# Kernel optimization log

Measured on AMD Instinct MI355X. Metric: run time of the kernel, lower is better.

## Reference

```python
import jax, jax.numpy as jnp
import numpy as np

B, N, F, A = 8, 2048, 512, 512  # batch, n_dim (tokens), feature_dim, attention_dim
BN_EPS = 1e-5


def setup_inputs() -> dict:
    key = jax.random.key(0)
    ks = jax.random.split(key, 9)
    s_f = 1.0 / np.sqrt(F)
    s_a = 1.0 / np.sqrt(A)
    return {
        "x": jax.random.normal(ks[0], (B, N, F), dtype=jnp.float32),
        "Wq": jax.random.uniform(ks[1], (A, F), jnp.float32, -s_f, s_f),
        "bq": jax.random.uniform(ks[2], (A,), jnp.float32, -s_f, s_f),
        "Wk": jax.random.uniform(ks[3], (A, F), jnp.float32, -s_f, s_f),
        "bk": jax.random.uniform(ks[4], (A,), jnp.float32, -s_f, s_f),
        "Wv": jax.random.uniform(ks[5], (A, F), jnp.float32, -s_f, s_f),
        "bv": jax.random.uniform(ks[6], (A,), jnp.float32, -s_f, s_f),
        "Wo": jax.random.uniform(ks[7], (F, A), jnp.float32, -s_a, s_a),
        "bo": jax.random.uniform(ks[8], (F,), jnp.float32, -s_a, s_a),
        "gamma": jnp.ones((N,), dtype=jnp.float32),
        "beta": jnp.zeros((N,), dtype=jnp.float32),
    }


def reference(x, Wq, bq, Wk, bk, Wv, bv, Wo, bo, gamma, beta):
    # QKV projections: [B,N,F] -> [B,N,A]
    q = jnp.einsum("bnf,af->bna", x, Wq) + bq
    k = jnp.einsum("bnf,af->bna", x, Wk) + bk
    v = jnp.einsum("bnf,af->bna", x, Wv) + bv
    # unscaled single-head attention (no 1/sqrt(d) factor, matches source)
    scores = jnp.einsum("bna,bma->bnm", q, k)          # [B,N,N]
    weights = jax.nn.softmax(scores, axis=-1)
    feature = jnp.einsum("bnm,bma->bna", weights, v)    # [B,N,A]
    # LBR: Linear -> BatchNorm1d(n_dim) over channel dim N -> ReLU
    lin = jnp.einsum("bna,fa->bnf", feature, Wo) + bo   # [B,N,F]
    mean = jnp.mean(lin, axis=(0, 2), keepdims=True)    # stats over batch+last dim
    var = jnp.mean(jnp.square(lin - mean), axis=(0, 2), keepdims=True)  # biased var
    bn = gamma[None, :, None] * (lin - mean) * jax.lax.rsqrt(var + BN_EPS) + beta[None, :, None]
    return jax.nn.relu(bn) + x
```

## Files before the change

kernel.cpp:

```cpp
#include <hip/hip_runtime.h>
#include <hip/hip_fp16.h>
#include <stdint.h>

#define B_   8
#define N_   2048
#define F_   512
#define A_   512
#define MTOT (B_ * N_)

typedef unsigned short u16;
typedef unsigned int   u32;
typedef __attribute__((ext_vector_type(8))) __bf16    bf16x8;
typedef __attribute__((ext_vector_type(8))) _Float16  f16x8;
typedef __attribute__((ext_vector_type(4))) float     f32x4;

__device__ __forceinline__ u16 f2bf(float f) {
    u32 u = __builtin_bit_cast(u32, f);
    u32 r = u + 0x7fffu + ((u >> 16) & 1u);
    return (u16)(r >> 16);
}
__device__ __forceinline__ u16 f2h(float f) {
    _Float16 h = (_Float16)f;
    return __builtin_bit_cast(u16, h);
}

__device__ __forceinline__ void gload_lds16(const u16* g, u16* l) {
    __builtin_amdgcn_global_load_lds(
        (const __attribute__((address_space(1))) u32*)(const u32*)g,
        (__attribute__((address_space(3))) u32*)(u32*)l,
        16, 0, 0);
}

template <int FMT>
__global__ __launch_bounds__(256) void cvt16(const float* __restrict__ in,
                                             u16* __restrict__ out, int n4) {
    int i = blockIdx.x * 256 + threadIdx.x;
    if (i >= n4) return;
    float4 v = ((const float4*)in)[i];
    u32 a, b;
    if constexpr (FMT == 0) {
        a = (u32)f2bf(v.x) | ((u32)f2bf(v.y) << 16);
        b = (u32)f2bf(v.z) | ((u32)f2bf(v.w) << 16);
    } else {
        a = (u32)f2h(v.x) | ((u32)f2h(v.y) << 16);
        b = (u32)f2h(v.z) | ((u32)f2h(v.w) << 16);
    }
    ((uint2*)out)[i] = make_uint2(a, b);
}

template <int BIAS_MODE, int OUT_FMT, int IN_FMT>
__global__ __launch_bounds__(256)
void gemm_nt(const u16* __restrict__ A, int lda, long sA,
             const u16* __restrict__ Bm, int ldb, long sB,
             const float* __restrict__ bias,
             void* __restrict__ Cv, int ldc, long sC, int K)
{
    __shared__ alignas(16) u16 lA[128 * 64];
    __shared__ alignas(16) u16 lB[128 * 64];

    const int z = blockIdx.z;
    A  += (long)z * sA;
    Bm += (long)z * sB;

    const int m0 = blockIdx.x * 128;
    const int n0 = blockIdx.y * 128;
    const int t = threadIdx.x;
    const int lane = t & 63, wave = t >> 6;
    const int wr = (wave >> 1) * 64;
    const int wc = (wave & 1) * 64;
    const int frow = lane & 15;
    const int fk   = (lane >> 4) * 8;

    f32x4 acc[4][4];
#pragma unroll
    for (int i = 0; i < 4; i++)
#pragma unroll
        for (int j = 0; j < 4; j++)
#pragma unroll
            for (int r = 0; r < 4; r++) acc[i][j][r] = 0.f;

    const int srow = t >> 3;
    const int scol = (t & 7) * 8;

    for (int kt = 0; kt < K; kt += 64) {
        __syncthreads();
#pragma unroll
        for (int s = 0; s < 4; ++s) {
            int row = s * 32 + srow;
            const u16* ga = A  + (long)(m0 + row) * lda + (kt + scol);
            const u16* gb = Bm + (long)(n0 + row) * ldb + (kt + scol);
            gload_lds16(ga, &lA[s * 2048 + t * 8]);
            gload_lds16(gb, &lB[s * 2048 + t * 8]);
        }
        __syncthreads();
#pragma unroll
        for (int kk = 0; kk < 64; kk += 32) {
            uint4 ar[4], br[4];
#pragma unroll
            for (int i = 0; i < 4; i++)
                ar[i] = *(const uint4*)&lA[(wr + i * 16 + frow) * 64 + kk + fk];
#pragma unroll
            for (int j = 0; j < 4; j++)
                br[j] = *(const uint4*)&lB[(wc + j * 16 + frow) * 64 + kk + fk];
#pragma unroll
            for (int i = 0; i < 4; i++)
#pragma unroll
                for (int j = 0; j < 4; j++) {
                    if constexpr (IN_FMT == 0)
                        acc[i][j] = __builtin_amdgcn_mfma_f32_16x16x32_bf16(
                            __builtin_bit_cast(bf16x8, ar[i]),
                            __builtin_bit_cast(bf16x8, br[j]),
                            acc[i][j], 0, 0, 0);
                    else
                        acc[i][j] = __builtin_amdgcn_mfma_f32_16x16x32_f16(
                            __builtin_bit_cast(f16x8, ar[i]),
                            __builtin_bit_cast(f16x8, br[j]),
                            acc[i][j], 0, 0, 0);
                }
        }
    }

    const int rbase = (lane >> 4) * 4;
#pragma unroll
    for (int i = 0; i < 4; i++) {
        int m = m0 + wr + i * 16 + rbase;
#pragma unroll
        for (int j = 0; j < 4; j++) {
            int n = n0 + wc + j * 16 + frow;
            float badd = 0.f;
            if (BIAS_MODE == 1) badd = bias[n];
#pragma unroll
            for (int r = 0; r < 4; r++) {
                float v = acc[i][j][r];
                if (BIAS_MODE == 1) v += badd;
                if (BIAS_MODE == 2) v += bias[m + r];
                long idx = (long)(m + r) * ldc + n + (long)z * sC;
                if constexpr (OUT_FMT == 0) {
                    ((u16*)Cv)[idx] = f2bf(v);
                } else if constexpr (OUT_FMT == 1) {
                    ((float*)Cv)[idx] = v;
                } else {
                    ((u16*)Cv)[idx] = f2h(v);
                }
            }
        }
    }
}

__global__ __launch_bounds__(256) void softmax_rows(u16* __restrict__ S) {
    __shared__ float red[16];
    const long row = blockIdx.x;
    u16* p = S + row * (long)N_;
    const int t = threadIdx.x;
    const int lane = t & 63, wave = t >> 6;

    uint4 raw = ((const uint4*)p)[t];
    const __half2* hp = (const __half2*)&raw;
    float v[8];
#pragma unroll
    for (int j = 0; j < 4; j++) {
        float2 f = __half22float2(hp[j]);
        v[2 * j]     = f.x;
        v[2 * j + 1] = f.y;
    }
    float mx = v[0];
#pragma unroll
    for (int j = 1; j < 8; j++) mx = fmaxf(mx, v[j]);
#pragma unroll
    for (int o = 32; o; o >>= 1) mx = fmaxf(mx, __shfl_xor(mx, o));
    if (lane == 0) red[wave] = mx;
    __syncthreads();
    mx = fmaxf(fmaxf(red[0], red[1]), fmaxf(red[2], red[3]));

    float s = 0.f;
#pragma unroll
    for (int j = 0; j < 8; j++) { v[j] = __expf(v[j] - mx); s += v[j]; }
#pragma unroll
    for (int o = 32; o; o >>= 1) s += __shfl_xor(s, o);
    if (lane == 0) red[8 + wave] = s;
    __syncthreads();
    s = red[8] + red[9] + red[10] + red[11];
    float inv = 1.f / s;
    u32 w[4];
#pragma unroll
    for (int j = 0; j < 4; j++) {
        u32 lo = f2bf(v[2 * j] * inv);
        u32 hi = f2bf(v[2 * j + 1] * inv);
        w[j] = lo | (hi << 16);
    }
    ((uint4*)p)[t] = make_uint4(w[0], w[1], w[2], w[3]);
}

__global__ __launch_bounds__(256) void bn_stats(const float* __restrict__ lin,
                                                float* __restrict__ stats) {
    __shared__ float red[16];
    const int n = blockIdx.x;
    const int t = threadIdx.x;
    const int lane = t & 63, wave = t >> 6;
    float s = 0.f, s2 = 0.f;
    for (int idx = t; idx < 1024; idx += 256) {
        int b = idx >> 7, f4 = idx & 127;
        float4 x = ((const float4*)(lin + ((long)b * N_ + n) * F_))[f4];
        s  += x.x + x.y + x.z + x.w;
        s2 += x.x * x.x + x.y * x.y + x.z * x.z + x.w * x.w;
    }
#pragma unroll
    for (int o = 32; o; o >>= 1) { s += __shfl_xor(s, o); s2 += __shfl_xor(s2, o); }
    if (lane == 0) { red[wave] = s; red[8 + wave] = s2; }
    __syncthreads();
    if (t == 0) {
        float S1 = red[0] + red[1] + red[2] + red[3];
        float S2 = red[8] + red[9] + red[10] + red[11];
        float mean = S1 / 4096.f;
        float var  = S2 / 4096.f - mean * mean;
        stats[n]      = mean;
        stats[N_ + n] = rsqrtf(var + 1e-5f);
    }
}

__global__ __launch_bounds__(256)
void bn_relu_add(const float* __restrict__ lin, const float* __restrict__ x,
                 const float* __restrict__ gamma, const float* __restrict__ beta,
                 const float* __restrict__ stats, float* __restrict__ out) {
    long i4 = (long)blockIdx.x * 256 + threadIdx.x;
    int n = (int)((i4 >> 7) & (N_ - 1));
    float mean = stats[n], rstd = stats[N_ + n];
    float scale = gamma[n] * rstd;
    float shift = beta[n] - mean * scale;
    float4 l  = ((const float4*)lin)[i4];
    float4 xx = ((const float4*)x)[i4];
    float4 o;
    o.x = fmaxf(l.x * scale + shift, 0.f) + xx.x;
    o.y = fmaxf(l.y * scale + shift, 0.f) + xx.y;
    o.z = fmaxf(l.z * scale + shift, 0.f) + xx.z;
    o.w = fmaxf(l.w * scale + shift, 0.f) + xx.w;
    ((float4*)out)[i4] = o;
}

extern "C" void kernel_launch(void* const* d_in, const int* in_sizes, int n_in,
                              void* d_out, int out_size, void* d_ws, size_t ws_size,
                              hipStream_t stream)
{
    (void)in_sizes; (void)n_in; (void)out_size; (void)ws_size;
    const float* x     = (const float*)d_in[0];
    const float* Wq    = (const float*)d_in[1];
    const float* bq    = (const float*)d_in[2];
    const float* Wk    = (const float*)d_in[3];
    const float* bk    = (const float*)d_in[4];
    const float* Wv    = (const float*)d_in[5];
    const float* bv    = (const float*)d_in[6];
    const float* Wo    = (const float*)d_in[7];
    const float* bo    = (const float*)d_in[8];
    const float* gamma = (const float*)d_in[9];
    const float* beta  = (const float*)d_in[10];
    float* out = (float*)d_out;
    char*  ws  = (char*)d_ws;

    const size_t MB = 1024 * 1024;
    u16*   wqkh  = (u16*)(ws + 0);
    u16*   wvh   = (u16*)(ws + 1 * MB);
    u16*   wob   = (u16*)(ws + 1 * MB + 512 * 1024);
    float* stats = (float*)(ws + 2 * MB);
    float* bqk   = (float*)(ws + 2 * MB + 64 * 1024);
    u16*   xh    = (u16*)(ws + 4 * MB);
    u16*   qkh   = (u16*)(ws + 20 * MB);
    u16*   vt    = (u16*)(ws + 52 * MB);
    u16*   S     = (u16*)(ws + 68 * MB);
    u16*   feat  = (u16*)(ws + 132 * MB);
    float* lin   = (float*)(ws + 148 * MB);

    hipMemcpyAsync(bqk,       bq, 512 * sizeof(float), hipMemcpyDeviceToDevice, stream);
    hipMemcpyAsync(bqk + 512, bk, 512 * sizeof(float), hipMemcpyDeviceToDevice, stream);

    cvt16<1><<<8192, 256, 0, stream>>>(x,  xh,  2097152);
    cvt16<1><<<256,  256, 0, stream>>>(Wq, wqkh,          65536);
    cvt16<1><<<256,  256, 0, stream>>>(Wk, wqkh + 262144, 65536);
    cvt16<1><<<256,  256, 0, stream>>>(Wv, wvh, 65536);
    cvt16<0><<<256,  256, 0, stream>>>(Wo, wob, 65536);

    gemm_nt<1, 2, 1><<<dim3(128, 8, 1), 256, 0, stream>>>(
        xh, 512, 0, wqkh, 512, 0, bqk, qkh, 1024, 0, 512);
    gemm_nt<2, 0, 1><<<dim3(4, 128, 1), 256, 0, stream>>>(
        wvh, 512, 0, xh, 512, 0, bv, vt, MTOT, 0, 512);

    gemm_nt<0, 2, 1><<<dim3(16, 16, 8), 256, 0, stream>>>(
        qkh, 1024, (long)N_ * 1024,
        qkh + 512, 1024, (long)N_ * 1024,
        nullptr, S, N_, (long)N_ * N_, 512);
    softmax_rows<<<MTOT, 256, 0, stream>>>(S);
    gemm_nt<0, 0, 0><<<dim3(16, 4, 8), 256, 0, stream>>>(
        S, N_, (long)N_ * N_,
        vt, MTOT, (long)N_,
        nullptr, feat, A_, (long)N_ * A_, 2048);

    gemm_nt<1, 1, 0><<<dim3(128, 4, 1), 256, 0, stream>>>(
        feat, 512, 0, wob, 512, 0, bo, lin, 512, 0, 512);
    bn_stats<<<2048, 256, 0, stream>>>(lin, stats);
    bn_relu_add<<<8192, 256, 0, stream>>>(lin, x, gamma, beta, stats, out);
}
```

Baseline: 245.6 us.

## Add 8-wave 256x256 pipelined fp16 GEMM for QK projection and scores

Introduces a new 512-thread GEMM kernel with 256x256 output tiles, a 4-stage LDS ring buffer fed by direct global-to-LDS loads, explicit vmcnt waits, and interleaved MFMA halves with priority bumps. It replaces the generic 128x128 GEMM for the fused Q/K projection and the batched QK^T score computation. The aim is more data reuse per tile and better overlap of memory loads with MFMA work. In exchange it uses 128KB of LDS and many accumulator registers, which limits occupancy to one block per CU and gives a coarser grid.

```diff
diff --git a/kernel.cpp b/kernel.cpp
--- a/kernel.cpp
+++ b/kernel.cpp
@@ -46,6 +46,119 @@
         b = (u32)f2h(v.z) | ((u32)f2h(v.w) << 16);
     }
     ((uint2*)out)[i] = make_uint2(a, b);
+}
+
+template <int BIAS_MODE>
+__global__ __launch_bounds__(512)
+void gemm8p(const u16* __restrict__ A, int lda, long sA,
+            const u16* __restrict__ Bm, int ldb, long sB,
+            const float* __restrict__ bias,
+            u16* __restrict__ C, int ldc, long sC, int K)
+{
+    __shared__ alignas(16) u16 lds8[65536];
+
+    const int z = blockIdx.z;
+    const int m0 = blockIdx.x * 256;
+    const int n0 = blockIdx.y * 256;
+    const u16* Ag = A  + (long)z * sA + (long)m0 * lda;
+    const u16* Bg = Bm + (long)z * sB + (long)n0 * ldb;
+
+    const int t = threadIdx.x;
+    const int lane = t & 63, wave = t >> 6;
+    const int wm = wave >> 2;
+    const int wn = wave & 3;
+    const int frow = lane & 15;
+    const int fkel = (lane >> 4) * 8;
+
+    const int NT = K >> 5;
+
+    auto stage2 = [&](const u16* g, int ld, int kel, u16* lbase) {
+#pragma unroll
+        for (int r = 0; r < 2; ++r) {
+            int row = r * 128 + (t >> 2);
+            int cel = ((t & 3) * 8) ^ ((row & 3) << 3);
+            gload_lds16(g + (long)row * ld + kel + cel, lbase + r * 4096 + t * 8);
+        }
+    };
+    auto rd = [&](int base, int row) -> uint4 {
+        return *(const uint4*)&lds8[base + row * 32 + (fkel ^ ((row & 3) << 3))];
+    };
+
+    f32x4 acc[8][4];
+#pragma unroll
+    for (int i = 0; i < 8; i++)
+#pragma unroll
+        for (int j = 0; j < 4; j++)
+#pragma unroll
+            for (int r = 0; r < 4; r++) acc[i][j][r] = 0.f;
+
+#pragma unroll
+    for (int T = 0; T < 3; ++T) {
+        stage2(Ag, lda, T * 32, &lds8[T * 16384]);
+        stage2(Bg, ldb, T * 32, &lds8[T * 16384 + 8192]);
+    }
+
+    for (int T = 0; T < NT; ++T) {
+        const int s  = (T & 3) * 16384;
+        const int sn = ((T + 3) & 3) * 16384;
+        const bool st = (T + 3 < NT);
+        const int kel = (T + 3) * 32;
+
+        if (T < NT - 2)      asm volatile("s_waitcnt vmcnt(8)" ::: "memory");
+        else if (T == NT - 2) asm volatile("s_waitcnt vmcnt(4)" ::: "memory");
+        else                 asm volatile("s_waitcnt vmcnt(0)" ::: "memory");
+        __builtin_amdgcn_sched_barrier(0);
+        __builtin_amdgcn_s_barrier();
+        __builtin_amdgcn_sched_barrier(0);
+
+        uint4 ar[4], br[4];
+#pragma unroll
+        for (int i = 0; i < 4; i++) ar[i] = rd(s, wm * 128 + i * 16 + frow);
+#pragma unroll
+        for (int j = 0; j < 4; j++) br[j] = rd(s + 8192, wn * 64 + j * 16 + frow);
+        if (st) stage2(Ag, lda, kel, &lds8[sn]);
+        __builtin_amdgcn_s_setprio(1);
+#pragma unroll
+        for (int i = 0; i < 4; i++)
+#pragma unroll
+            for (int j = 0; j < 4; j++)
+                acc[i][j] = __builtin_amdgcn_mfma_f32_16x16x32_f16(
+                    __builtin_bit_cast(f16x8, ar[i]),
+                    __builtin_bit_cast(f16x8, br[j]), acc[i][j], 0, 0, 0);
+        __builtin_amdgcn_s_setprio(0);
+        __builtin_amdgcn_sched_barrier(0);
+        __builtin_amdgcn_s_barrier();
+        __builtin_amdgcn_sched_barrier(0);
+
+        uint4 ar2[4];
+#pragma unroll
+        for (int i = 0; i < 4; i++) ar2[i] = rd(s, wm * 128 + 64 + i * 16 + frow);
+        if (st) stage2(Bg, ldb, kel, &lds8[sn + 8192]);
+        __builtin_amdgcn_s_setprio(1);
+#pragma unroll
+        for (int i = 0; i < 4; i++)
+#pragma unroll
+            for (int j = 0; j < 4; j++)
+                acc[4 + i][j] = __builtin_amdgcn_mfma_f32_16x16x32_f16(
+                    __builtin_bit_cast(f16x8, ar2[i]),
+                    __builtin_bit_cast(f16x8, br[j]), acc[4 + i][j], 0, 0, 0);
+        __builtin_amdgcn_s_setprio(0);
+    }
+
+    const int q4 = (lane >> 4) * 4;
+#pragma unroll
+    for (int ii = 0; ii < 8; ii++) {
+        int m = m0 + wm * 128 + (ii >> 2) * 64 + (ii & 3) * 16 + q4;
+#pragma unroll
+        for (int j = 0; j < 4; j++) {
+            int n = n0 + wn * 64 + j * 16 + frow;
+            float badd = 0.f;
+            if (BIAS_MODE == 1) badd = bias[n];
+#pragma unroll
+            for (int r = 0; r < 4; r++)
+                C[(long)(m + r) * ldc + n + (long)z * sC] = f2h(acc[ii][j][r] + badd);
+        }
+    }
 }
 
 template <int BIAS_MODE, int OUT_FMT, int IN_FMT>
@@ -278,12 +391,12 @@
     cvt16<1><<<256,  256, 0, stream>>>(Wv, wvh, 65536);
     cvt16<0><<<256,  256, 0, stream>>>(Wo, wob, 65536);
 
-    gemm_nt<1, 2, 1><<<dim3(128, 8, 1), 256, 0, stream>>>(
+    gemm8p<1><<<dim3(64, 4, 1), 512, 0, stream>>>(
         xh, 512, 0, wqkh, 512, 0, bqk, qkh, 1024, 0, 512);
     gemm_nt<2, 0, 1><<<dim3(4, 128, 1), 256, 0, stream>>>(
         wvh, 512, 0, xh, 512, 0, bv, vt, MTOT, 0, 512);
 
-    gemm_nt<0, 2, 1><<<dim3(16, 16, 8), 256, 0, stream>>>(
+    gemm8p<0><<<dim3(8, 8, 8), 512, 0, stream>>>(
         qkh, 1024, (long)N_ * 1024,
         qkh + 512, 1024, (long)N_ * 1024,
         nullptr, S, N_, (long)N_ * N_, 512);
```

Result: faster. 238.7 us (-2.8%).

## Replace GEMM with 256-row, 8-wave, double-buffered, swizzled LDS pipelined kernel

Applied to the files above, without the earlier changes.

Replaces the 128x128 single-buffered GEMM with a 512-thread kernel using 256xBN tiles, double-buffered LDS with an XOR swizzle, and staged global-to-LDS loads interleaved with MFMA phases under explicit vmcnt waits, barriers and setprio. The aim is to hide global-load latency, cut LDS bank conflicts and raise the compute-to-load ratio. The PV GEMM now folds the batch into M through a diagonal B offset instead of grid z. The risks are higher register and LDS pressure and fragile hand-tuned wait counts.

```diff
diff --git a/kernel.cpp b/kernel.cpp
--- a/kernel.cpp
+++ b/kernel.cpp
@@ -29,6 +29,19 @@
         (const __attribute__((address_space(1))) u32*)(const u32*)g,
         (__attribute__((address_space(3))) u32*)(u32*)l,
         16, 0, 0);
+}
+
+#define VMCNT(n) asm volatile("s_waitcnt vmcnt(" #n ")" ::: "memory")
+
+__device__ __forceinline__ void sync_pre() {
+    __builtin_amdgcn_sched_barrier(0);
+    __builtin_amdgcn_s_barrier();
+    asm volatile("s_waitcnt lgkmcnt(0)" ::: "memory");
+    __builtin_amdgcn_sched_barrier(0);
+}
+__device__ __forceinline__ void sync_post() {
+    __builtin_amdgcn_sched_barrier(0);
+    __builtin_amdgcn_s_barrier();
 }
 
 template <int FMT>
@@ -48,100 +61,202 @@
     ((uint2*)out)[i] = make_uint2(a, b);
 }
 
-template <int BIAS_MODE, int OUT_FMT, int IN_FMT>
-__global__ __launch_bounds__(256)
-void gemm_nt(const u16* __restrict__ A, int lda, long sA,
-             const u16* __restrict__ Bm, int ldb, long sB,
-             const float* __restrict__ bias,
-             void* __restrict__ Cv, int ldc, long sC, int K)
+template <int BN, int BIAS_MODE, int OUT_FMT, int IN_FMT>
+__global__ __launch_bounds__(512, 2)
+void gemm8(const u16* __restrict__ A, int lda, long sA,
+           const u16* __restrict__ Bm, int ldb, long sB,
+           const float* __restrict__ bias,
+           void* __restrict__ Cv, int ldc, long sC, int K, int bdiag)
 {
-    __shared__ alignas(16) u16 lA[128 * 64];
-    __shared__ alignas(16) u16 lB[128 * 64];
-
-    const int z = blockIdx.z;
-    A  += (long)z * sA;
-    Bm += (long)z * sB;
-
-    const int m0 = blockIdx.x * 128;
-    const int n0 = blockIdx.y * 128;
+    constexpr int UNITS = (BN == 256) ? 4 : 3;
+    constexpr int NF = BN / 64;
+    __shared__ alignas(16) u16 lds[2 * UNITS * 8192];
+
+    const int z  = blockIdx.z;
+    const int m0 = blockIdx.x * 256;
+    const int n0 = blockIdx.y * BN;
+    const u16* Ag = A  + (long)z * sA + (long)m0 * lda;
+    const u16* Bg = Bm + (long)z * sB + (long)n0 * ldb + (long)(m0 >> 11) * bdiag;
+
     const int t = threadIdx.x;
-    const int lane = t & 63, wave = t >> 6;
-    const int wr = (wave >> 1) * 64;
-    const int wc = (wave & 1) * 64;
+    const int lane = t & 63;
+    const int wave = t >> 6;
+    const int wm = wave >> 2, wn = wave & 3;
     const int frow = lane & 15;
-    const int fk   = (lane >> 4) * 8;
-
-    f32x4 acc[4][4];
-#pragma unroll
-    for (int i = 0; i < 4; i++)
-#pragma unroll
-        for (int j = 0; j < 4; j++)
+    const int fk8 = (lane >> 4) * 8;
+
+    const int srr = t >> 3;
+    const int ses = ((t & 7) * 8) ^ ((srr & 7) << 3);
+
+    auto stageA = [&](int buf, int h, int kt) {
+        u16* dst = &lds[(buf * UNITS + h) * 8192 + t * 8];
+        const u16* g = Ag + kt * 64 + ses;
+        gload_lds16(g + (long)(srr + h * 64) * lda,        dst);
+        gload_lds16(g + (long)(srr + 128 + h * 64) * lda,  dst + 4096);
+    };
+    auto stageB = [&](int buf, int h, int kt) {
+        u16* dst = &lds[(buf * UNITS + 2 + h) * 8192 + t * 8];
+        const u16* g = Bg + kt * 64 + ses;
+        int R0;
+        if constexpr (BN == 256) R0 = (srr & 31) + ((srr >> 5) << 6) + h * 32;
+        else                     R0 = srr;
+        int R1 = R0 + ((BN == 256) ? 128 : 64);
+        gload_lds16(g + (long)R0 * ldb, dst);
+        gload_lds16(g + (long)R1 * ldb, dst + 4096);
+    };
+    auto rdA = [&](int buf, int q, int i, int ks) -> uint4 {
+        int rr = wm * 64 + i * 16 + frow;
+        int e  = (ks * 32 + fk8) ^ ((rr & 7) << 3);
+        return *(const uint4*)&lds[(buf * UNITS + q) * 8192 + rr * 64 + e];
+    };
+    auto rdB = [&](int buf, int p, int j, int ks) -> uint4 {
+        int rr = wn * 32 + j * 16 + frow;
+        int e  = (ks * 32 + fk8) ^ ((rr & 7) << 3);
+        return *(const uint4*)&lds[(buf * UNITS + 2 + p) * 8192 + rr * 64 + e];
+    };
+    auto MF = [&](uint4 a, uint4 b, f32x4 c) -> f32x4 {
+        if constexpr (IN_FMT == 0)
+            return __builtin_amdgcn_mfma_f32_16x16x32_bf16(
+                __builtin_bit_cast(bf16x8, a), __builtin_bit_cast(bf16x8, b), c, 0, 0, 0);
+        else
+            return __builtin_amdgcn_mfma_f32_16x16x32_f16(
+                __builtin_bit_cast(f16x8, a), __builtin_bit_cast(f16x8, b), c, 0, 0, 0);
+    };
+
+    f32x4 acc[8][NF];
+#pragma unroll
+    for (int i = 0; i < 8; i++)
+#pragma unroll
+        for (int j = 0; j < NF; j++)
 #pragma unroll
             for (int r = 0; r < 4; r++) acc[i][j][r] = 0.f;
 
-    const int srow = t >> 3;
-    const int scol = (t & 7) * 8;
-
-    for (int kt = 0; kt < K; kt += 64) {
-        __syncthreads();
-#pragma unroll
-        for (int s = 0; s < 4; ++s) {
-            int row = s * 32 + srow;
-            const u16* ga = A  + (long)(m0 + row) * lda + (kt + scol);
-            const u16* gb = Bm + (long)(n0 + row) * ldb + (kt + scol);
-            gload_lds16(ga, &lA[s * 2048 + t * 8]);
-            gload_lds16(gb, &lB[s * 2048 + t * 8]);
+    uint4 fa[4][2], fb0[2][2], fb1[2][2];
+    const int NT = K >> 6;
+
+    if constexpr (BN == 256) {
+        stageA(0, 0, 0); stageB(0, 0, 0); stageB(0, 1, 0); stageA(0, 1, 0);
+        VMCNT(4);
+    } else {
+        stageA(0, 0, 0); stageB(0, 0, 0); stageA(0, 1, 0);
+        VMCNT(2);
+    }
+    __builtin_amdgcn_sched_barrier(0);
+    __builtin_amdgcn_s_barrier();
+
+    for (int kt = 0; kt < NT; ++kt) {
+        const int buf = kt & 1, nb = buf ^ 1;
+        const bool st = (kt + 1 < NT);
+
+        if constexpr (BN == 256) {
+#pragma unroll
+            for (int i = 0; i < 4; i++) { fa[i][0] = rdA(buf, 0, i, 0); fa[i][1] = rdA(buf, 0, i, 1); }
+#pragma unroll
+            for (int j = 0; j < 2; j++) { fb0[j][0] = rdB(buf, 0, j, 0); fb0[j][1] = rdB(buf, 0, j, 1); }
+            if (st) { stageA(nb, 0, kt + 1); VMCNT(4); } else VMCNT(2);
+            sync_pre();
+            __builtin_amdgcn_s_setprio(1);
+#pragma unroll
+            for (int ks = 0; ks < 2; ks++)
+#pragma unroll
+                for (int i = 0; i < 4; i++)
+#pragma unroll
+                    for (int j = 0; j < 2; j++)
+                        acc[i][j] = MF(fa[i][ks], fb0[j][ks], acc[i][j]);
+            __builtin_amdgcn_s_setprio(0);
+            sync_post();
+#pragma unroll
+            for (int j = 0; j < 2; j++) { fb1[j][0] = rdB(buf, 1, j, 0); fb1[j][1] = rdB(buf, 1, j, 1); }
+            if (st) { stageB(nb, 0, kt + 1); VMCNT(4); } else VMCNT(0);
+            sync_pre();
+            __builtin_amdgcn_s_setprio(1);
+#pragma unroll
+            for (int ks = 0; ks < 2; ks++)
+#pragma unroll
+                for (int i = 0; i < 4; i++)
+#pragma unroll
+                    for (int j = 0; j < 2; j++)
+                        acc[i][2 + j] = MF(fa[i][ks], fb1[j][ks], acc[i][2 + j]);
+            __builtin_amdgcn_s_setprio(0);
+            sync_post();
+#pragma unroll
+            for (int i = 0; i < 4; i++) { fa[i][0] = rdA(buf, 1, i, 0); fa[i][1] = rdA(buf, 1, i, 1); }
+            if (st) stageB(nb, 1, kt + 1);
+            sync_pre();
+            __builtin_amdgcn_s_setprio(1);
+#pragma unroll
+            for (int ks = 0; ks < 2; ks++)
+#pragma unroll
+                for (int i = 0; i < 4; i++)
+#pragma unroll
+                    for (int j = 0; j < 2; j++)
+                        acc[4 + i][j] = MF(fa[i][ks], fb0[j][ks], acc[4 + i][j]);
+            __builtin_amdgcn_s_setprio(0);
+            sync_post();
+            if (st) { stageA(nb, 1, kt + 1); VMCNT(4); }
+            sync_pre();
+            __builtin_amdgcn_s_setprio(1);
+#pragma unroll
+            for (int ks = 0; ks < 2; ks++)
+#pragma unroll
+                for (int i = 0; i < 4; i++)
+#pragma unroll
+                    for (int j = 0; j < 2; j++)
+                        acc[4 + i][2 + j] = MF(fa[i][ks], fb1[j][ks], acc[4 + i][2 + j]);
+            __builtin_amdgcn_s_setprio(0);
+            sync_post();
+        } else {
+#pragma unroll
+            for (int i = 0; i < 4; i++) { fa[i][0] = rdA(buf, 0, i, 0); fa[i][1] = rdA(buf, 0, i, 1); }
+#pragma unroll
+            for (int j = 0; j < 2; j++) { fb0[j][0] = rdB(buf, 0, j, 0); fb0[j][1] = rdB(buf, 0, j, 1); }
+            if (st) { stageA(nb, 0, kt + 1); stageB(nb, 0, kt + 1); VMCNT(4); } else VMCNT(0);
+            sync_pre();
+            __builtin_amdgcn_s_setprio(1);
+#pragma unroll
+            for (int ks = 0; ks < 2; ks++)
+#pragma unroll
+                for (int i = 0; i < 4; i++)
+#pragma unroll
+                    for (int j = 0; j < 2; j++)
+                        acc[i][j] = MF(fa[i][ks], fb0[j][ks], acc[i][j]);
+            __builtin_amdgcn_s_setprio(0);
+            sync_post();
+#pragma unroll
+            for (int i = 0; i < 4; i++) { fa[i][0] = rdA(buf, 1, i, 0); fa[i][1] = rdA(buf, 1, i, 1); }
+            if (st) { stageA(nb, 1, kt + 1); VMCNT(2); }
+            sync_pre();
+            __builtin_amdgcn_s_setprio(1);
+#pragma unroll
+            for (int ks = 0; ks < 2; ks++)
+#pragma unroll
+                for (int i = 0; i < 4; i++)
+#pragma unroll
+                    for (int j = 0; j < 2; j++)
+                        acc[4 + i][j] = MF(fa[i][ks], fb0[j][ks], acc[4 + i][j]);
+            __builtin_amdgcn_s_setprio(0);
+            sync_post();
         }
-        __syncthreads();
-#pragma unroll
-        for (int kk = 0; kk < 64; kk += 32) {
-            uint4 ar[4], br[4];
-#pragma unroll
-            for (int i = 0; i < 4; i++)
-                ar[i] = *(const uint4*)&lA[(wr + i * 16 + frow) * 64 + kk + fk];
-#pragma unroll
-            for (int j = 0; j < 4; j++)
-                br[j] = *(const uint4*)&lB[(wc + j * 16 + frow) * 64 + kk + fk];
-#pragma unroll
-            for (int i = 0; i < 4; i++)
-#pragma unroll
-                for (int j = 0; j < 4; j++) {
-                    if constexpr (IN_FMT == 0)
-                        acc[i][j] = __builtin_amdgcn_mfma_f32_16x16x32_bf16(
-                            __builtin_bit_cast(bf16x8, ar[i]),
-                            __builtin_bit_cast(bf16x8, br[j]),
-                            acc[i][j], 0, 0, 0);
-                    else
-                        acc[i][j] = __builtin_amdgcn_mfma_f32_16x16x32_f16(
-                            __builtin_bit_cast(f16x8, ar[i]),
-                            __builtin_bit_cast(f16x8, br[j]),
-                            acc[i][j], 0, 0, 0);
-                }
-        }
-    }
-
-    const int rbase = (lane >> 4) * 4;
-#pragma unroll
-    for (int i = 0; i < 4; i++) {
-        int m = m0 + wr + i * 16 + rbase;
-#pragma unroll
-        for (int j = 0; j < 4; j++) {
-            int n = n0 + wc + j * 16 + frow;
+    }
+
+    const int rq = (lane >> 4) * 4;
+#pragma unroll
+    for (int am = 0; am < 8; am++) {
+        const int m = m0 + wm * 128 + (am >> 2) * 64 + (am & 3) * 16 + rq;
+#pragma unroll
+        for (int an = 0; an < NF; an++) {
+            const int n = n0 + wn * (BN / 4) + an * 16 + frow;
             float badd = 0.f;
             if (BIAS_MODE == 1) badd = bias[n];
 #pragma unroll
             for (int r = 0; r < 4; r++) {
-                float v = acc[i][j][r];
+                float v = acc[am][an][r];
                 if (BIAS_MODE == 1) v += badd;
                 if (BIAS_MODE == 2) v += bias[m + r];
                 long idx = (long)(m + r) * ldc + n + (long)z * sC;
-                if constexpr (OUT_FMT == 0) {
-                    ((u16*)Cv)[idx] = f2bf(v);
-                } else if constexpr (OUT_FMT == 1) {
-                    ((float*)Cv)[idx] = v;
-                } else {
-                    ((u16*)Cv)[idx] = f2h(v);
-                }
+                if constexpr (OUT_FMT == 0)      ((u16*)Cv)[idx] = f2bf(v);
+                else if constexpr (OUT_FMT == 1) ((float*)Cv)[idx] = v;
+                else                             ((u16*)Cv)[idx] = f2h(v);
             }
         }
     }
@@ -278,23 +393,19 @@
     cvt16<1><<<256,  256, 0, stream>>>(Wv, wvh, 65536);
     cvt16<0><<<256,  256, 0, stream>>>(Wo, wob, 65536);
 
-    gemm_nt<1, 2, 1><<<dim3(128, 8, 1), 256, 0, stream>>>(
-        xh, 512, 0, wqkh, 512, 0, bqk, qkh, 1024, 0, 512);
-    gemm_nt<2, 0, 1><<<dim3(4, 128, 1), 256, 0, stream>>>(
-        wvh, 512, 0, xh, 512, 0, bv, vt, MTOT, 0, 512);
-
-    gemm_nt<0, 2, 1><<<dim3(16, 16, 8), 256, 0, stream>>>(
-        qkh, 1024, (long)N_ * 1024,
-        qkh + 512, 1024, (long)N_ * 1024,
-        nullptr, S, N_, (long)N_ * N_, 512);
+    gemm8<256, 1, 2, 1><<<dim3(64, 4, 1), 512, 0, stream>>>(
+        xh, 512, 0, wqkh, 512, 0, bqk, qkh, 1024, 0, 512, 0);
+    gemm8<128, 2, 0, 1><<<dim3(2, 128, 1), 512, 0, stream>>>(
+        wvh, 512, 0, xh, 512, 0, bv, vt, MTOT, 0, 512, 0);
+    gemm8<256, 0, 2, 1><<<dim3(8, 8, 8), 512, 0, stream>>>(
+        qkh, 1024, (long)N_ * 1024, qkh + 512, 1024, (long)N_ * 1024,
+        nullptr, S, N_, (long)N_ * N_, 512, 0);
     softmax_rows<<<MTOT, 256, 0, stream>>>(S);
-    gemm_nt<0, 0, 0><<<dim3(16, 4, 8), 256, 0, stream>>>(
-        S, N_, (long)N_ * N_,
-        vt, MTOT, (long)N_,
-        nullptr, feat, A_, (long)N_ * A_, 2048);
-
-    gemm_nt<1, 1, 0><<<dim3(128, 4, 1), 256, 0, stream>>>(
-        feat, 512, 0, wob, 512, 0, bo, lin, 512, 0, 512);
+    gemm8<128, 0, 0, 0><<<dim3(64, 4, 1), 512, 0, stream>>>(
+        S, N_, 0, vt, MTOT, 0, nullptr, feat, A_, 0, 2048, 2048);
+    gemm8<128, 1, 1, 0><<<dim3(64, 4, 1), 512, 0, stream>>>(
+        feat, 512, 0, wob, 512, 0, bo, lin, 512, 0, 512, 0);
+
     bn_stats<<<2048, 256, 0, stream>>>(lin, stats);
     bn_relu_add<<<8192, 256, 0, stream>>>(lin, x, gamma, beta, stats, out);
 }
```

Result: faster. 214.2 us (-12.8%).

## Pipeline GEMM with triple-buffered LDS, swizzled layout, and fused BN stats

Applied to the files above, without the earlier changes.

Replaces the GEMM kernel with a triple-buffered, K-step-32 pipeline that keeps prefetching global-to-LDS loads in flight under explicit vmcnt waits. It also XOR-swizzles the LDS layout to reduce bank conflicts and changes the wave tiling so each wave owns 128x32. BatchNorm statistics are now accumulated in the output-projection GEMM epilogue with atomics, removing the separate bn_stats pass over lin. The attention-value GEMM batch index is folded into the grid via a diagonal offset. The trade-offs are more hand-tuned scheduling and atomic contention on the stats buffer.

```diff
diff --git a/kernel.cpp b/kernel.cpp
--- a/kernel.cpp
+++ b/kernel.cpp
@@ -30,6 +30,10 @@
         (__attribute__((address_space(3))) u32*)(u32*)l,
         16, 0, 0);
 }
+
+#define VMCNT(n) asm volatile("s_waitcnt vmcnt(" #n ")" ::: "memory")
+#define LGKM0()  asm volatile("s_waitcnt lgkmcnt(0)" ::: "memory")
+#define SCHEDB() __builtin_amdgcn_sched_barrier(0)
 
 template <int FMT>
 __global__ __launch_bounds__(256) void cvt16(const float* __restrict__ in,
@@ -48,99 +52,140 @@
     ((uint2*)out)[i] = make_uint2(a, b);
 }
 
-template <int BIAS_MODE, int OUT_FMT, int IN_FMT>
-__global__ __launch_bounds__(256)
-void gemm_nt(const u16* __restrict__ A, int lda, long sA,
-             const u16* __restrict__ Bm, int ldb, long sB,
-             const float* __restrict__ bias,
-             void* __restrict__ Cv, int ldc, long sC, int K)
+template <int BIAS_MODE, int OUT_FMT, int IN_FMT, int STATS>
+__global__ __launch_bounds__(256, 3)
+void gemmp(const u16* __restrict__ A, int lda, long sA,
+           const u16* __restrict__ Bm, int ldb, long sB,
+           const float* __restrict__ bias,
+           void* __restrict__ Cv, int ldc, long sC, int K, int bdiag,
+           float* __restrict__ stats)
 {
-    __shared__ alignas(16) u16 lA[128 * 64];
-    __shared__ alignas(16) u16 lB[128 * 64];
-
-    const int z = blockIdx.z;
-    A  += (long)z * sA;
-    Bm += (long)z * sB;
-
+    __shared__ alignas(16) u16 lds[3][2][4096];
+
+    const int z  = blockIdx.z;
     const int m0 = blockIdx.x * 128;
     const int n0 = blockIdx.y * 128;
+    const u16* Ag = A  + (long)z * sA + (long)m0 * lda;
+    const u16* Bg = Bm + (long)z * sB + (long)n0 * ldb + (long)(m0 >> 11) * bdiag;
+
     const int t = threadIdx.x;
-    const int lane = t & 63, wave = t >> 6;
-    const int wr = (wave >> 1) * 64;
-    const int wc = (wave & 1) * 64;
+    const int lane = t & 63;
+    const int wn   = t >> 6;
     const int frow = lane & 15;
-    const int fk   = (lane >> 4) * 8;
-
-    f32x4 acc[4][4];
-#pragma unroll
-    for (int i = 0; i < 4; i++)
-#pragma unroll
-        for (int j = 0; j < 4; j++)
+    const int fk8  = (lane >> 4) * 8;
+
+    const int sr = t >> 2;
+    const int se = ((t & 3) * 8) ^ ((sr & 3) << 3);
+
+    auto stage = [&](int slot, int unit, const u16* g, int ld, int kel) {
+        u16* dst = &lds[slot][unit][t * 8];
+        const u16* gp = g + kel + se;
+        gload_lds16(gp + (long)sr * ld,        dst);
+        gload_lds16(gp + (long)(sr + 64) * ld, dst + 2048);
+    };
+    auto rd = [&](int slot, int unit, int row) -> uint4 {
+        return *(const uint4*)&lds[slot][unit][row * 32 + (fk8 ^ ((row & 3) << 3))];
+    };
+    auto MF = [&](uint4 a, uint4 b, f32x4 c) -> f32x4 {
+        if constexpr (IN_FMT == 0)
+            return __builtin_amdgcn_mfma_f32_16x16x32_bf16(
+                __builtin_bit_cast(bf16x8, a), __builtin_bit_cast(bf16x8, b), c, 0, 0, 0);
+        else
+            return __builtin_amdgcn_mfma_f32_16x16x32_f16(
+                __builtin_bit_cast(f16x8, a), __builtin_bit_cast(f16x8, b), c, 0, 0, 0);
+    };
+
+    f32x4 acc[8][2];
+#pragma unroll
+    for (int i = 0; i < 8; i++)
+#pragma unroll
+        for (int j = 0; j < 2; j++)
 #pragma unroll
             for (int r = 0; r < 4; r++) acc[i][j][r] = 0.f;
 
-    const int srow = t >> 3;
-    const int scol = (t & 7) * 8;
-
-    for (int kt = 0; kt < K; kt += 64) {
-        __syncthreads();
-#pragma unroll
-        for (int s = 0; s < 4; ++s) {
-            int row = s * 32 + srow;
-            const u16* ga = A  + (long)(m0 + row) * lda + (kt + scol);
-            const u16* gb = Bm + (long)(n0 + row) * ldb + (kt + scol);
-            gload_lds16(ga, &lA[s * 2048 + t * 8]);
-            gload_lds16(gb, &lB[s * 2048 + t * 8]);
+    const int NT = K >> 5;
+
+    stage(0, 0, Ag, lda, 0);  stage(0, 1, Bg, ldb, 0);
+    stage(1, 0, Ag, lda, 32); stage(1, 1, Bg, ldb, 32);
+
+    int bc = 0, b1 = 1, b2 = 2;
+    uint4 fa[4], fb[2];
+
+    for (int kt = 0; kt < NT; ++kt) {
+        const bool st2 = (kt + 2 < NT);
+        const int kel2 = (kt + 2) << 5;
+
+        if (st2) {
+            stage(b2, 0, Ag, lda, kel2);
+            VMCNT(6);
+        } else if (kt + 2 == NT) {
+            VMCNT(4);
+        } else {
+            VMCNT(0);
         }
-        __syncthreads();
-#pragma unroll
-        for (int kk = 0; kk < 64; kk += 32) {
-            uint4 ar[4], br[4];
-#pragma unroll
-            for (int i = 0; i < 4; i++)
-                ar[i] = *(const uint4*)&lA[(wr + i * 16 + frow) * 64 + kk + fk];
-#pragma unroll
-            for (int j = 0; j < 4; j++)
-                br[j] = *(const uint4*)&lB[(wc + j * 16 + frow) * 64 + kk + fk];
-#pragma unroll
-            for (int i = 0; i < 4; i++)
-#pragma unroll
-                for (int j = 0; j < 4; j++) {
-                    if constexpr (IN_FMT == 0)
-                        acc[i][j] = __builtin_amdgcn_mfma_f32_16x16x32_bf16(
-                            __builtin_bit_cast(bf16x8, ar[i]),
-                            __builtin_bit_cast(bf16x8, br[j]),
-                            acc[i][j], 0, 0, 0);
-                    else
-                        acc[i][j] = __builtin_amdgcn_mfma_f32_16x16x32_f16(
-                            __builtin_bit_cast(f16x8, ar[i]),
-                            __builtin_bit_cast(f16x8, br[j]),
-                            acc[i][j], 0, 0, 0);
+        SCHEDB();
+        __builtin_amdgcn_s_barrier();
+        SCHEDB();
+#pragma unroll
+        for (int i = 0; i < 4; i++) fa[i] = rd(bc, 0, i * 16 + frow);
+        fb[0] = rd(bc, 1, wn * 32 + frow);
+        fb[1] = rd(bc, 1, wn * 32 + 16 + frow);
+        LGKM0(); SCHEDB();
+        __builtin_amdgcn_s_setprio(1);
+#pragma unroll
+        for (int i = 0; i < 4; i++)
+#pragma unroll
+            for (int j = 0; j < 2; j++)
+                acc[i][j] = MF(fa[i], fb[j], acc[i][j]);
+        __builtin_amdgcn_s_setprio(0);
+
+        if (st2) stage(b2, 1, Bg, ldb, kel2);
+#pragma unroll
+        for (int i = 0; i < 4; i++) fa[i] = rd(bc, 0, 64 + i * 16 + frow);
+        LGKM0(); SCHEDB();
+        __builtin_amdgcn_s_setprio(1);
+#pragma unroll
+        for (int i = 0; i < 4; i++)
+#pragma unroll
+            for (int j = 0; j < 2; j++)
+                acc[4 + i][j] = MF(fa[i], fb[j], acc[4 + i][j]);
+        __builtin_amdgcn_s_setprio(0);
+        SCHEDB();
+        __builtin_amdgcn_s_barrier();
+        int tmp = bc; bc = b1; b1 = b2; b2 = tmp;
+    }
+
+    const int rq = (lane >> 4) * 4;
+#pragma unroll
+    for (int am = 0; am < 8; am++) {
+        const int m = m0 + am * 16 + rq;
+#pragma unroll
+        for (int r = 0; r < 4; r++) {
+            float vv[2];
+#pragma unroll
+            for (int an = 0; an < 2; an++) {
+                const int n = n0 + wn * 32 + an * 16 + frow;
+                float v = acc[am][an][r];
+                if (BIAS_MODE == 1) v += bias[n];
+                if (BIAS_MODE == 2) v += bias[m + r];
+                vv[an] = v;
+                long idx = (long)(m + r) * ldc + n + (long)z * sC;
+                if constexpr (OUT_FMT == 0)      ((u16*)Cv)[idx] = f2bf(v);
+                else if constexpr (OUT_FMT == 1) ((float*)Cv)[idx] = v;
+                else                             ((u16*)Cv)[idx] = f2h(v);
+            }
+            if constexpr (STATS) {
+                float s1 = vv[0] + vv[1];
+                float s2 = vv[0] * vv[0] + vv[1] * vv[1];
+#pragma unroll
+                for (int o = 1; o < 16; o <<= 1) {
+                    s1 += __shfl_xor(s1, o);
+                    s2 += __shfl_xor(s2, o);
                 }
-        }
-    }
-
-    const int rbase = (lane >> 4) * 4;
-#pragma unroll
-    for (int i = 0; i < 4; i++) {
-        int m = m0 + wr + i * 16 + rbase;
-#pragma unroll
-        for (int j = 0; j < 4; j++) {
-            int n = n0 + wc + j * 16 + frow;
-            float badd = 0.f;
-            if (BIAS_MODE == 1) badd = bias[n];
-#pragma unroll
-            for (int r = 0; r < 4; r++) {
-                float v = acc[i][j][r];
-                if (BIAS_MODE == 1) v += badd;
-                if (BIAS_MODE == 2) v += bias[m + r];
-                long idx = (long)(m + r) * ldc + n + (long)z * sC;
-                if constexpr (OUT_FMT == 0) {
-                    ((u16*)Cv)[idx] = f2bf(v);
-                } else if constexpr (OUT_FMT == 1) {
-                    ((float*)Cv)[idx] = v;
-                } else {
-                    ((u16*)Cv)[idx] = f2h(v);
+                if (frow == 0) {
+                    int tok = (m + r) & (N_ - 1);
+                    atomicAdd(&stats[tok], s1);
+                    atomicAdd(&stats[N_ + tok], s2);
                 }
             }
         }
@@ -191,40 +236,15 @@
     ((uint4*)p)[t] = make_uint4(w[0], w[1], w[2], w[3]);
 }
 
-__global__ __launch_bounds__(256) void bn_stats(const float* __restrict__ lin,
-                                                float* __restrict__ stats) {
-    __shared__ float red[16];
-    const int n = blockIdx.x;
-    const int t = threadIdx.x;
-    const int lane = t & 63, wave = t >> 6;
-    float s = 0.f, s2 = 0.f;
-    for (int idx = t; idx < 1024; idx += 256) {
-        int b = idx >> 7, f4 = idx & 127;
-        float4 x = ((const float4*)(lin + ((long)b * N_ + n) * F_))[f4];
-        s  += x.x + x.y + x.z + x.w;
-        s2 += x.x * x.x + x.y * x.y + x.z * x.z + x.w * x.w;
-    }
-#pragma unroll
-    for (int o = 32; o; o >>= 1) { s += __shfl_xor(s, o); s2 += __shfl_xor(s2, o); }
-    if (lane == 0) { red[wave] = s; red[8 + wave] = s2; }
-    __syncthreads();
-    if (t == 0) {
-        float S1 = red[0] + red[1] + red[2] + red[3];
-        float S2 = red[8] + red[9] + red[10] + red[11];
-        float mean = S1 / 4096.f;
-        float var  = S2 / 4096.f - mean * mean;
-        stats[n]      = mean;
-        stats[N_ + n] = rsqrtf(var + 1e-5f);
-    }
-}
-
 __global__ __launch_bounds__(256)
 void bn_relu_add(const float* __restrict__ lin, const float* __restrict__ x,
                  const float* __restrict__ gamma, const float* __restrict__ beta,
                  const float* __restrict__ stats, float* __restrict__ out) {
     long i4 = (long)blockIdx.x * 256 + threadIdx.x;
     int n = (int)((i4 >> 7) & (N_ - 1));
-    float mean = stats[n], rstd = stats[N_ + n];
+    float mean = stats[n] * (1.f / 4096.f);
+    float var  = stats[N_ + n] * (1.f / 4096.f) - mean * mean;
+    float rstd = rsqrtf(var + 1e-5f);
     float scale = gamma[n] * rstd;
     float shift = beta[n] - mean * scale;
     float4 l  = ((const float4*)lin)[i4];
@@ -269,6 +289,7 @@
     u16*   feat  = (u16*)(ws + 132 * MB);
     float* lin   = (float*)(ws + 148 * MB);
 
+    hipMemsetAsync(stats, 0, 2 * N_ * sizeof(float), stream);
     hipMemcpyAsync(bqk,       bq, 512 * sizeof(float), hipMemcpyDeviceToDevice, stream);
     hipMemcpyAsync(bqk + 512, bk, 512 * sizeof(float), hipMemcpyDeviceToDevice, stream);
 
@@ -278,23 +299,18 @@
     cvt16<1><<<256,  256, 0, stream>>>(Wv, wvh, 65536);
     cvt16<0><<<256,  256, 0, stream>>>(Wo, wob, 65536);
 
-    gemm_nt<1, 2, 1><<<dim3(128, 8, 1), 256, 0, stream>>>(
-        xh, 512, 0, wqkh, 512, 0, bqk, qkh, 1024, 0, 512);
-    gemm_nt<2, 0, 1><<<dim3(4, 128, 1), 256, 0, stream>>>(
-        wvh, 512, 0, xh, 512, 0, bv, vt, MTOT, 0, 512);
-
-    gemm_nt<0, 2, 1><<<dim3(16, 16, 8), 256, 0, stream>>>(
-        qkh, 1024, (long)N_ * 1024,
-        qkh + 512, 1024, (long)N_ * 1024,
-        nullptr, S, N_, (long)N_ * N_, 512);
+    gemmp<1, 2, 1, 0><<<dim3(128, 8, 1), 256, 0, stream>>>(
+        xh, 512, 0, wqkh, 512, 0, bqk, qkh, 1024, 0, 512, 0, nullptr);
+    gemmp<2, 0, 1, 0><<<dim3(4, 128, 1), 256, 0, stream>>>(
+        wvh, 512, 0, xh, 512, 0, bv, vt, MTOT, 0, 512, 0, nullptr);
+    gemmp<0, 2, 1, 0><<<dim3(16, 16, 8), 256, 0, stream>>>(
+        qkh, 1024, (long)N_ * 1024, qkh + 512, 1024, (long)N_ * 1024,
+        nullptr, S, N_, (long)N_ * N_, 512, 0, nullptr);
     softmax_rows<<<MTOT, 256, 0, stream>>>(S);
-    gemm_nt<0, 0, 0><<<dim3(16, 4, 8), 256, 0, stream>>>(
-        S, N_, (long)N_ * N_,
-        vt, MTOT, (long)N_,
-        nullptr, feat, A_, (long)N_ * A_, 2048);
-
-    gemm_nt<1, 1, 0><<<dim3(128, 4, 1), 256, 0, stream>>>(
-        feat, 512, 0, wob, 512, 0, bo, lin, 512, 0, 512);
-    bn_stats<<<2048, 256, 0, stream>>>(lin, stats);
+    gemmp<0, 0, 0, 0><<<dim3(128, 4, 1), 256, 0, stream>>>(
+        S, N_, 0, vt, MTOT, 0, nullptr, feat, A_, 0, 2048, 2048, nullptr);
+    gemmp<1, 1, 0, 1><<<dim3(128, 4, 1), 256, 0, stream>>>(
+        feat, 512, 0, wob, 512, 0, bo, lin, 512, 0, 512, 0, stats);
+
     bn_relu_add<<<8192, 256, 0, stream>>>(lin, x, gamma, beta, stats, out);
 }
```

After: 287.4 us. 1.17x slower.
